# Kernel optimization log

Measured on AMD Instinct MI355X. Metric: run time of the kernel, lower is better.

## Reference

```python
import jax, jax.numpy as jnp
import numpy as np

HEADS = 12
WINDOW = 128

def setup_inputs() -> dict:
    key = jax.random.key(0)
    ks = jax.random.split(key, 5)
    B, N, C = 1, 4096, 768
    return {
        'x': jax.random.normal(ks[0], (B, N, C), dtype=jnp.float32),
        'qkv_w': jax.random.normal(ks[1], (3 * C, C), dtype=jnp.float32) * 0.02,
        'qkv_b': jax.random.normal(ks[2], (3 * C,), dtype=jnp.float32) * 0.02,
        'proj_w': jax.random.normal(ks[3], (C, C), dtype=jnp.float32) * 0.02,
        'proj_b': jax.random.normal(ks[4], (C,), dtype=jnp.float32) * 0.02,
    }

def reference(x, qkv_w, qkv_b, proj_w, proj_b):
    B, N, C = x.shape
    H = HEADS
    hd = C // H
    # qkv projection (torch Linear: y = x @ W^T + b)
    qkv = x @ qkv_w.T + qkv_b                      # [B, N, 3C]
    qkv = qkv.reshape(B, N, 3, H, hd).transpose(2, 0, 3, 1, 4)  # [3, B, H, N, hd]
    q, k, v = qkv[0], qkv[1], qkv[2]               # each [B, H, N, hd]
    # local (banded) mask: |i - j| <= window_size
    idxs = jnp.arange(N)
    local = jnp.abs(idxs[:, None] - idxs[None, :]) <= WINDOW  # [N, N] bool
    # dense scores then mask (faithful to original O(N^2) math)
    attn = jnp.einsum('bhnd,bhmd->bhnm', q, k) / jnp.sqrt(jnp.float32(hd))
    attn = jnp.where(local[None, None], attn, -jnp.inf)
    attn = jax.nn.softmax(attn, axis=-1)
    out = jnp.einsum('bhnm,bhmd->bhnd', attn, v)   # [B, H, N, hd]
    out = out.transpose(0, 2, 1, 3).reshape(B, N, C)
    return out @ proj_w.T + proj_b
```

## Files before the change

kernel.cpp:

```cpp
#include <hip/hip_runtime.h>
#include <hip/hip_fp16.h>
#include <cmath>

typedef _Float16 f16;
typedef __attribute__((ext_vector_type(8))) _Float16 f16x8;
typedef __attribute__((ext_vector_type(4))) _Float16 f16x4;
typedef __attribute__((ext_vector_type(4))) float f32x4;

typedef __attribute__((address_space(3))) unsigned int lds_u32;
typedef const __attribute__((address_space(1))) unsigned int g_u32;
__device__ __forceinline__ void async_copy16(const void* g, void* l) {
    __builtin_amdgcn_global_load_lds((g_u32*)g, (lds_u32*)l, 16, 0, 0);
}

#define EXP2F(x) __builtin_amdgcn_exp2f(x)

__global__ void cast3_f32_f16(const float* __restrict__ s0, f16* __restrict__ d0, int n0,
                              const float* __restrict__ s1, f16* __restrict__ d1, int n1,
                              const float* __restrict__ s2, f16* __restrict__ d2, int n2) {
    int i = blockIdx.x * blockDim.x + threadIdx.x;
    const float* s; f16* d; int j;
    if (i < n0)                { s = s0; d = d0; j = i; }
    else if (i < n0 + n1)      { s = s1; d = d1; j = i - n0; }
    else if (i < n0 + n1 + n2) { s = s2; d = d2; j = i - n0 - n1; }
    else return;
    float4 v = ((const float4*)s)[j];
    f16x4 o = { (f16)v.x, (f16)v.y, (f16)v.z, (f16)v.w };
    ((f16x4*)d)[j] = o;
}

__device__ __forceinline__ void store4(f16* p, const f32x4& v) {
    f16x4 o = { (f16)v[0], (f16)v[1], (f16)v[2], (f16)v[3] };
    *(f16x4*)p = o;
}
__device__ __forceinline__ void store4(float* p, const f32x4& v) {
    float4 o = { v[0], v[1], v[2], v[3] };
    *(float4*)p = o;
}

template <int BN_T, typename OT>
__global__ __launch_bounds__(256) void gemm_f16_nt_db(
    const f16* __restrict__ A,
    const f16* __restrict__ W,
    const float* __restrict__ bias,
    OT* __restrict__ out,
    int M, int N, int K)
{
    constexpr int NCH = BN_T / 16;
    constexpr int NT  = BN_T / 64;
    __shared__ f16 Ash[2][4 * 512];
    __shared__ f16 Bsh[2][NCH * 512];

    const int tid  = threadIdx.x;
    const int lane = tid & 63;
    const int w    = tid >> 6;
    const int lr   = lane & 15;
    const int lq   = lane >> 4;
    const int bm   = blockIdx.y * 64;
    const int bn   = blockIdx.x * BN_T;

    const f16* gA = A + (size_t)(bm + w * 16 + lr) * K + lq * 8;
    const f16* gB[NT];
#pragma unroll
    for (int t = 0; t < NT; ++t)
        gB[t] = W + (size_t)(bn + (w * NT + t) * 16 + lr) * K + lq * 8;

    f32x4 acc[4][NT] = {};

    async_copy16(gA, &Ash[0][w * 512]);
#pragma unroll
    for (int t = 0; t < NT; ++t)
        async_copy16(gB[t], &Bsh[0][(w * NT + t) * 512]);
    __syncthreads();

    const int nk = K >> 5;
    for (int k = 0; k < nk; ++k) {
        const int cur = k & 1;
        if (k + 1 < nk) {
            int ko = (k + 1) << 5;
            async_copy16(gA + ko, &Ash[cur ^ 1][w * 512]);
#pragma unroll
            for (int t = 0; t < NT; ++t)
                async_copy16(gB[t] + ko, &Bsh[cur ^ 1][(w * NT + t) * 512]);
        }
        f16x8 af[4], bf[NT];
#pragma unroll
        for (int mt = 0; mt < 4; ++mt)
            af[mt] = *(const f16x8*)&Ash[cur][mt * 512 + lane * 8];
#pragma unroll
        for (int nt = 0; nt < NT; ++nt)
            bf[nt] = *(const f16x8*)&Bsh[cur][(w * NT + nt) * 512 + lane * 8];
#pragma unroll
        for (int mt = 0; mt < 4; ++mt)
#pragma unroll
            for (int nt = 0; nt < NT; ++nt)
                acc[mt][nt] = __builtin_amdgcn_mfma_f32_16x16x32_f16(
                    bf[nt], af[mt], acc[mt][nt], 0, 0, 0);
        __syncthreads();
    }

#pragma unroll
    for (int mt = 0; mt < 4; ++mt) {
        int row = bm + mt * 16 + lr;
#pragma unroll
        for (int nt = 0; nt < NT; ++nt) {
            int col = bn + (w * NT + nt) * 16 + lq * 4;
            float4 bv = *(const float4*)(bias + col);
            f32x4 ov = acc[mt][nt];
            ov[0] += bv.x; ov[1] += bv.y; ov[2] += bv.z; ov[3] += bv.w;
            store4(out + (size_t)row * N + col, ov);
        }
    }
}

#define WINDOW_SZ 128

__global__ __launch_bounds__(256) void local_attn_mfma(
    const f16* __restrict__ qkv,
    f16* __restrict__ out,
    int N)
{
    const int C  = 768;
    const int C3 = 2304;
    __shared__ f16 Ks[8 * 512];
    __shared__ f16 Vt[4096];
    __shared__ f16 Ps[8 * 512];

    const int tid  = threadIdx.x;
    const int lane = tid & 63;
    const int w    = tid >> 6;
    const int r15  = lane & 15;
    const int q4   = lane >> 4;
    const int ntiles = N >> 6;
    const int h  = blockIdx.x / ntiles;
    const int i0 = (blockIdx.x % ntiles) << 6;
    const int qoff = h * 64;
    const int koff = 768 + h * 64;
    const int voff = 1536 + h * 64;

    f16x8 qf[2];
    {
        const f16* qrow = qkv + (size_t)(i0 + w * 16 + r15) * C3 + qoff + q4 * 8;
        qf[0] = *(const f16x8*)(qrow);
        qf[1] = *(const f16x8*)(qrow + 32);
        const f16 qs = (f16)0.18033688f;
#pragma unroll
        for (int j = 0; j < 8; ++j) { qf[0][j] *= qs; qf[1][j] *= qs; }
    }

    const int vc0 = tid >> 3;
    const int vd0 = (tid & 7) * 8;
    const int va  = vd0 >> 3;

    f32x4 o[4] = {};
    float m_l = -1.0e30f, l_l = 0.f;

    for (int ch = 0; ch < 5; ++ch) {
        int jbase = i0 - 128 + ch * 64;
        if (jbase < 0 || jbase >= N) continue;
        bool need_mask = (ch == 0) || (ch == 4);

        __syncthreads();
        {
            const f16* kr = qkv + (size_t)(jbase + w * 16 + r15) * C3 + koff + q4 * 8;
            async_copy16(kr,      &Ks[(w * 2 + 0) * 512]);
            async_copy16(kr + 32, &Ks[(w * 2 + 1) * 512]);
        }
#pragma unroll
        for (int rep = 0; rep < 2; ++rep) {
            int c = vc0 + rep * 32;
            f16x8 v = *(const f16x8*)(qkv + (size_t)(jbase + c) * C3 + voff + vd0);
            int cc = c >> 3, c7 = c & 7;
#pragma unroll
            for (int j = 0; j < 8; ++j) {
                int x = (cc ^ va ^ j) & 7;
                Vt[(vd0 + j) * 64 + x * 8 + c7] = v[j];
            }
        }
        __syncthreads();

        f32x4 s[4] = {};
#pragma unroll
        for (int ks = 0; ks < 2; ++ks)
#pragma unroll
            for (int nt = 0; nt < 4; ++nt) {
                f16x8 kf = *(const f16x8*)&Ks[(nt * 2 + ks) * 512 + lane * 8];
                s[nt] = __builtin_amdgcn_mfma_f32_16x16x32_f16(kf, qf[ks], s[nt], 0, 0, 0);
            }

        if (need_mask) {
            int qg = i0 + w * 16 + r15;
#pragma unroll
            for (int nt = 0; nt < 4; ++nt)
#pragma unroll
                for (int r = 0; r < 4; ++r) {
                    int dist = qg - (jbase + nt * 16 + q4 * 4 + r);
                    if (dist < 0) dist = -dist;
                    if (dist > WINDOW_SZ) s[nt][r] = -3.0e38f;
                }
        }

        float rmax = -3.0e38f;
#pragma unroll
        for (int nt = 0; nt < 4; ++nt)
#pragma unroll
            for (int r = 0; r < 4; ++r) rmax = fmaxf(rmax, s[nt][r]);
        rmax = fmaxf(rmax, __shfl_xor(rmax, 16));
        rmax = fmaxf(rmax, __shfl_xor(rmax, 32));
        float mn = fmaxf(m_l, rmax);
        float al = EXP2F(m_l - mn);
        m_l = mn;
        float rs = 0.f;
#pragma unroll
        for (int nt = 0; nt < 4; ++nt)
#pragma unroll
            for (int r = 0; r < 4; ++r) {
                float p = EXP2F(s[nt][r] - mn);
                s[nt][r] = p;
                rs += p;
            }
        rs += __shfl_xor(rs, 16);
        rs += __shfl_xor(rs, 32);
        l_l = l_l * al + rs;
#pragma unroll
        for (int nd = 0; nd < 4; ++nd)
#pragma unroll
            for (int r = 0; r < 4; ++r) o[nd][r] *= al;

#pragma unroll
        for (int nt = 0; nt < 4; ++nt)
#pragma unroll
            for (int r = 0; r < 4; ++r) {
                int c  = nt * 16 + q4 * 4 + r;
                int cs = c >> 5;
                int c5 = c & 31;
                int ls = (c5 >> 3) * 16 + r15;
                int lss = ls ^ ((ls >> 3) & 7);
                Ps[(w * 2 + cs) * 512 + lss * 8 + (c5 & 7)] = (f16)s[nt][r];
            }

        int lssr = lane ^ ((lane >> 3) & 7);
#pragma unroll
        for (int cs = 0; cs < 2; ++cs) {
            f16x8 pf = *(const f16x8*)&Ps[(w * 2 + cs) * 512 + lssr * 8];
#pragma unroll
            for (int nd = 0; nd < 4; ++nd) {
                int d = nd * 16 + r15;
                int x = ((cs * 4 + q4) ^ (d >> 3) ^ d) & 7;
                f16x8 vf = *(const f16x8*)&Vt[d * 64 + x * 8];
                o[nd] = __builtin_amdgcn_mfma_f32_16x16x32_f16(vf, pf, o[nd], 0, 0, 0);
            }
        }
    }

    float inv = 1.0f / l_l;
    int row = i0 + w * 16 + r15;
#pragma unroll
    for (int nd = 0; nd < 4; ++nd) {
        f16x4 ov = { (f16)(o[nd][0] * inv), (f16)(o[nd][1] * inv),
                     (f16)(o[nd][2] * inv), (f16)(o[nd][3] * inv) };
        *(f16x4*)(out + (size_t)row * C + qoff + nd * 16 + q4 * 4) = ov;
    }
}

extern "C" void kernel_launch(void* const* d_in, const int* in_sizes, int n_in,
                              void* d_out, int out_size, void* d_ws, size_t ws_size,
                              hipStream_t stream) {
    (void)n_in; (void)out_size; (void)ws_size;
    const float* x      = (const float*)d_in[0];
    const float* qkv_w  = (const float*)d_in[1];
    const float* qkv_b  = (const float*)d_in[2];
    const float* proj_w = (const float*)d_in[3];
    const float* proj_b = (const float*)d_in[4];
    float* outp = (float*)d_out;

    const int C    = in_sizes[2] / 3;
    const int Nseq = in_sizes[0] / C;
    const int C3   = 3 * C;

    char* ws = (char*)d_ws;
    f16* qkv_h = (f16*)ws;   ws += (size_t)Nseq * C3 * 2;
    f16* xh    = (f16*)ws;   ws += (size_t)Nseq * C * 2;
    f16* wh_q  = (f16*)ws;   ws += (size_t)C3 * C * 2;
    f16* wh_p  = (f16*)ws;
    f16* attn_h = xh;

    dim3 blk(256);
    {
        int n0 = Nseq * C / 4, n1 = C3 * C / 4, n2 = C * C / 4;
        int tot = n0 + n1 + n2;
        cast3_f32_f16<<<dim3((tot + 255) / 256), blk, 0, stream>>>(
            x, xh, n0, qkv_w, wh_q, n1, proj_w, wh_p, n2);
    }
    gemm_f16_nt_db<128, f16><<<dim3(C3 / 128, Nseq / 64), blk, 0, stream>>>(
        xh, wh_q, qkv_b, qkv_h, Nseq, C3, C);
    local_attn_mfma<<<dim3((C / 64) * (Nseq / 64)), blk, 0, stream>>>(
        qkv_h, attn_h, Nseq);
    gemm_f16_nt_db<64, float><<<dim3(C / 64, Nseq / 64), blk, 0, stream>>>(
        attn_h, wh_p, proj_b, outp, Nseq, C, C);
}
```

Measured before the change: 163.1 us.

## Replace LDS-staged GEMM with register-streamed 2x2-warp GEMM loading directly from global

Measured after the change: 198.2 us. +21.5%, slower.

```diff
diff --git a/kernel.cpp b/kernel.cpp
--- a/kernel.cpp
+++ b/kernel.cpp
@@ -38,73 +38,79 @@
     *(float4*)p = o;
 }
 
-template <int BN_T, typename OT>
-__global__ __launch_bounds__(256) void gemm_f16_nt_db(
+template <int MT, int NT, typename OT>
+__global__ __launch_bounds__(256) void gemm_f16_stream(
     const f16* __restrict__ A,
     const f16* __restrict__ W,
     const float* __restrict__ bias,
     OT* __restrict__ out,
     int M, int N, int K)
 {
-    constexpr int NCH = BN_T / 16;
-    constexpr int NT  = BN_T / 64;
-    __shared__ f16 Ash[2][4 * 512];
-    __shared__ f16 Bsh[2][NCH * 512];
-
     const int tid  = threadIdx.x;
     const int lane = tid & 63;
     const int w    = tid >> 6;
+    const int wr   = w >> 1;
+    const int wc   = w & 1;
     const int lr   = lane & 15;
     const int lq   = lane >> 4;
-    const int bm   = blockIdx.y * 64;
-    const int bn   = blockIdx.x * BN_T;
-
-    const f16* gA = A + (size_t)(bm + w * 16 + lr) * K + lq * 8;
-    const f16* gB[NT];
-#pragma unroll
-    for (int t = 0; t < NT; ++t)
-        gB[t] = W + (size_t)(bn + (w * NT + t) * 16 + lr) * K + lq * 8;
-
-    f32x4 acc[4][NT] = {};
-
-    async_copy16(gA, &Ash[0][w * 512]);
-#pragma unroll
-    for (int t = 0; t < NT; ++t)
-        async_copy16(gB[t], &Bsh[0][(w * NT + t) * 512]);
-    __syncthreads();
+    const int bm   = blockIdx.y * (2 * MT * 16);
+    const int bn   = blockIdx.x * (2 * NT * 16);
+
+    const f16* pa[MT];
+    const f16* pb[NT];
+#pragma unroll
+    for (int mt = 0; mt < MT; ++mt)
+        pa[mt] = A + (size_t)(bm + wr * MT * 16 + mt * 16 + lr) * K + lq * 8;
+#pragma unroll
+    for (int nt = 0; nt < NT; ++nt)
+        pb[nt] = W + (size_t)(bn + wc * NT * 16 + nt * 16 + lr) * K + lq * 8;
+
+    f32x4 acc[MT][NT] = {};
+    f16x8 a0[MT], b0[NT], a1[MT], b1[NT];
+
+#pragma unroll
+    for (int mt = 0; mt < MT; ++mt) a0[mt] = *(const f16x8*)(pa[mt]);
+#pragma unroll
+    for (int nt = 0; nt < NT; ++nt) b0[nt] = *(const f16x8*)(pb[nt]);
 
     const int nk = K >> 5;
-    for (int k = 0; k < nk; ++k) {
-        const int cur = k & 1;
+    for (int k = 0; k < nk; k += 2) {
         if (k + 1 < nk) {
             int ko = (k + 1) << 5;
-            async_copy16(gA + ko, &Ash[cur ^ 1][w * 512]);
-#pragma unroll
-            for (int t = 0; t < NT; ++t)
-                async_copy16(gB[t] + ko, &Bsh[cur ^ 1][(w * NT + t) * 512]);
-        }
-        f16x8 af[4], bf[NT];
-#pragma unroll
-        for (int mt = 0; mt < 4; ++mt)
-            af[mt] = *(const f16x8*)&Ash[cur][mt * 512 + lane * 8];
-#pragma unroll
-        for (int nt = 0; nt < NT; ++nt)
-            bf[nt] = *(const f16x8*)&Bsh[cur][(w * NT + nt) * 512 + lane * 8];
-#pragma unroll
-        for (int mt = 0; mt < 4; ++mt)
+#pragma unroll
+            for (int mt = 0; mt < MT; ++mt) a1[mt] = *(const f16x8*)(pa[mt] + ko);
+#pragma unroll
+            for (int nt = 0; nt < NT; ++nt) b1[nt] = *(const f16x8*)(pb[nt] + ko);
+        }
+#pragma unroll
+        for (int mt = 0; mt < MT; ++mt)
 #pragma unroll
             for (int nt = 0; nt < NT; ++nt)
                 acc[mt][nt] = __builtin_amdgcn_mfma_f32_16x16x32_f16(
-                    bf[nt], af[mt], acc[mt][nt], 0, 0, 0);
-        __syncthreads();
-    }
-
-#pragma unroll
-    for (int mt = 0; mt < 4; ++mt) {
-        int row = bm + mt * 16 + lr;
+                    b0[nt], a0[mt], acc[mt][nt], 0, 0, 0);
+        if (k + 2 < nk) {
+            int ko = (k + 2) << 5;
+#pragma unroll
+            for (int mt = 0; mt < MT; ++mt) a0[mt] = *(const f16x8*)(pa[mt] + ko);
+#pragma unroll
+            for (int nt = 0; nt < NT; ++nt) b0[nt] = *(const f16x8*)(pb[nt] + ko);
+        }
+        if (k + 1 < nk) {
+#pragma unroll
+            for (int mt = 0; mt < MT; ++mt)
+#pragma unroll
+                for (int nt = 0; nt < NT; ++nt)
+                    acc[mt][nt] = __builtin_amdgcn_mfma_f32_16x16x32_f16(
+                        b1[nt], a1[mt], acc[mt][nt], 0, 0, 0);
+        }
+    }
+
+#pragma unroll
+    for (int mt = 0; mt < MT; ++mt) {
+        int row = bm + wr * MT * 16 + mt * 16 + lr;
 #pragma unroll
         for (int nt = 0; nt < NT; ++nt) {
-            int col = bn + (w * NT + nt) * 16 + lq * 4;
+            int col = bn + wc * NT * 16 + nt * 16 + lq * 4;
             float4 bv = *(const float4*)(bias + col);
             f32x4 ov = acc[mt][nt];
             ov[0] += bv.x; ov[1] += bv.y; ov[2] += bv.z; ov[3] += bv.w;
@@ -292,10 +298,10 @@
         cast3_f32_f16<<<dim3((tot + 255) / 256), blk, 0, stream>>>(
             x, xh, n0, qkv_w, wh_q, n1, proj_w, wh_p, n2);
     }
-    gemm_f16_nt_db<128, f16><<<dim3(C3 / 128, Nseq / 64), blk, 0, stream>>>(
+    gemm_f16_stream<4, 4, f16><<<dim3(C3 / 128, Nseq / 128), blk, 0, stream>>>(
         xh, wh_q, qkv_b, qkv_h, Nseq, C3, C);
     local_attn_mfma<<<dim3((C / 64) * (Nseq / 64)), blk, 0, stream>>>(
         qkv_h, attn_h, Nseq);
-    gemm_f16_nt_db<64, float><<<dim3(C / 64, Nseq / 64), blk, 0, stream>>>(
+    gemm_f16_stream<2, 2, float><<<dim3(C / 64, Nseq / 64), blk, 0, stream>>>(
         attn_h, wh_p, proj_b, outp, Nseq, C, C);
 }
```
